# Kernel tuning notes

Measured on AMD Instinct MI355X. Metric: run time of the kernel, lower is better.

## Reference

```python
import jax, jax.numpy as jnp
import numpy as np
from functools import partial

NUM_ITERS = 3
NUM_CAPS = 8      # primary capsule count
NUM_CLASSES = 10
OUT_CH = 16       # digit capsule dim
INPUT_SIZE = 32 * 6 * 6  # 1152 primary capsule units per capsule map


def squash(s, axis=-1):
    # faithful to non_linear_squashing: s * (||s||^2/(1+||s||^2)) / (||s||+1e-10)
    norm_sqr = jnp.sum(s * s, axis=axis, keepdims=True)
    scale = jnp.sqrt(norm_sqr) + 1e-10
    mag = norm_sqr / (1.0 + norm_sqr)
    return s * mag / scale


def conv2d(x, w, b, stride):
    y = jax.lax.conv_general_dilated(
        x, w, window_strides=(stride, stride), padding='VALID',
        dimension_numbers=('NCHW', 'OIHW', 'NCHW'))
    return y + b[None, :, None, None]


def setup_inputs() -> dict:
    key = jax.random.key(0)
    ks = jax.random.split(key, 6)
    B = 256
    x = jax.random.normal(ks[0], (B, 1, 28, 28), dtype=jnp.float32)
    conv_w = jax.random.normal(ks[1], (256, 1, 9, 9), dtype=jnp.float32) * 0.05
    conv_b = jax.random.normal(ks[2], (256,), dtype=jnp.float32) * 0.05
    # 8 primary capsule conv units (256->32 each) fused into one 256->256 conv
    prim_w = jax.random.normal(ks[3], (NUM_CAPS * 32, 256, 9, 9), dtype=jnp.float32) * 0.02
    prim_b = jax.random.normal(ks[4], (NUM_CAPS * 32,), dtype=jnp.float32) * 0.02
    # digit routing weights (input_size, num_classes, out_channels, num_capsules)
    digit_w = jax.random.normal(ks[5], (INPUT_SIZE, NUM_CLASSES, OUT_CH, NUM_CAPS), dtype=jnp.float32)
    return {'x': x, 'conv_w': conv_w, 'conv_b': conv_b,
            'prim_w': prim_w, 'prim_b': prim_b, 'digit_w': digit_w}


def reference(x, conv_w, conv_b, prim_w, prim_b, digit_w):
    B = x.shape[0]
    # conv stack: 1->256 k9 s1 + ReLU  (28 -> 20); pool is MaxPool2d(1,1) = identity
    h = jax.nn.relu(conv2d(x, conv_w, conv_b, stride=1))  # (B,256,20,20)
    # primary capsules: 8 convs 256->32 k9 s2, no activation (nl_activation=False)
    p = conv2d(h, prim_w, prim_b, stride=2)               # (B,256,6,6)
    u = p.reshape(B, NUM_CAPS, -1)                        # (B,8,1152)
    u = squash(u, axis=-1)
    # digit layer with dynamic routing
    # u_i: (B, IS, 8);  u_j_i[b,i,c,o] = sum_k W[i,c,o,k] * u_i[b,i,k]
    u_i = jnp.transpose(u, (0, 2, 1))                     # (B,1152,8)
    u_j_i = jnp.einsum('icok,bik->bico', digit_w, u_i)    # (B,1152,10,16)
    b_ij = jnp.zeros((INPUT_SIZE, NUM_CLASSES), dtype=x.dtype)
    out = None
    for _ in range(NUM_ITERS):
        c_ij = jax.nn.softmax(b_ij, axis=0)               # softmax over input capsules (dim=1 in torch)
        s_j = jnp.einsum('ic,bico->bco', c_ij, u_j_i)     # (B,10,16)
        # original squashes (B,1,C,16,1) along dim=2 == the CLASS axis
        out = squash(s_j, axis=1)                         # (B,10,16)
        # agreement: mean over batch of <u_j_i, v_j>
        u_v = jnp.einsum('bico,bco->ic', u_j_i, out) / B  # (1152,10)
        b_ij = b_ij + u_v
    # torch returns out.squeeze(1) with shape (B, C, 16, 1)
    return out[..., None]
```

## Files before the change

### kernel.cpp

```cpp
#include <hip/hip_runtime.h>
#include <cstdint>
#include <cstddef>


typedef __attribute__((ext_vector_type(8))) short short8;
typedef __attribute__((ext_vector_type(4))) float f32x4;

#define PHALF 2359296

__device__ __forceinline__ unsigned short f2bf_rn(float x) {
    unsigned u = __float_as_uint(x);
    unsigned r = (u + 0x7fffu + ((u >> 16) & 1u)) >> 16;
    return (unsigned short)r;
}

__global__ void k_makew(const float* __restrict__ w2,
                        unsigned short* __restrict__ wt) {
    __shared__ float lw[20736];
    int ocg = blockIdx.x, icg = blockIdx.y, t = threadIdx.x;
    for (int idx = t; idx < 20736; idx += 256) {
        int row = idx / 81, k = idx % 81;
        int oc_l = row >> 5, ic_l = row & 31;
        lw[idx] = w2[((size_t)(ocg * 8 + oc_l) * 256 + icg * 32 + ic_l) * 81 + k];
    }
    __syncthreads();
    for (int idx = t; idx < 2592; idx += 256) {
        int k = idx >> 5;
        int r = idx & 31;
        int oc_l = r >> 2, sl = r & 3;
        unsigned short hi8[8];
        #pragma unroll
        for (int j = 0; j < 8; j++)
            hi8[j] = f2bf_rn(lw[(oc_l * 32 + sl * 8 + j) * 81 + k]);
        size_t o = ((size_t)(k * 256 + ocg * 8 + oc_l)) * 256 + icg * 32 + sl * 8;
        *(uint4*)&wt[o] = *(uint4*)hi8;
    }
}

__global__ void k_conv1(const float* __restrict__ x, const float* __restrict__ cw,
                        const float* __restrict__ cb,
                        unsigned short* __restrict__ h) {
    __shared__ float img[784];
    __shared__ float wsm[32 * 81];
    int b = blockIdx.x, ocg = blockIdx.y, t = threadIdx.x;
    for (int idx = t; idx < 784; idx += 256) img[idx] = x[b * 784 + idx];
    for (int idx = t; idx < 2592; idx += 256) wsm[idx] = cw[ocg * 2592 + idx];
    __syncthreads();
    int oc_l = t & 31, g = t >> 5;
    int oc = ocg * 32 + oc_l;
    float bias = cb[oc];
    const float* wp = &wsm[oc_l * 81];
    for (int q = g; q < 100; q += 8) {
        int py = q / 5, qx = (q % 5) * 4;
        float a0 = bias, a1 = bias, a2 = bias, a3 = bias;
        #pragma unroll
        for (int ky = 0; ky < 9; ky++) {
            const float* ir = &img[(py + ky) * 28 + qx];
            float r[12];
            #pragma unroll
            for (int j = 0; j < 12; j++) r[j] = ir[j];
            #pragma unroll
            for (int kx = 0; kx < 9; kx++) {
                float w = wp[ky * 9 + kx];
                a0 += r[kx] * w; a1 += r[kx + 1] * w;
                a2 += r[kx + 2] * w; a3 += r[kx + 3] * w;
            }
        }
        float v[4] = { fmaxf(a0, 0.f), fmaxf(a1, 0.f), fmaxf(a2, 0.f), fmaxf(a3, 0.f) };
        size_t base = ((size_t)b * 400 + py * 20 + qx) * 256 + oc;
        #pragma unroll
        for (int j = 0; j < 4; j++)
            h[base + (size_t)j * 256] = f2bf_rn(v[j]);
    }
}

__global__ __launch_bounds__(256, 4) void k_conv2m(
    const unsigned short* __restrict__ h,
    const unsigned short* __restrict__ wt,
    float* __restrict__ p0, float* __restrict__ p1,
    float* __restrict__ p2, float* __restrict__ p3)
{
    __shared__ unsigned short smem[14336];
    const int t = threadIdx.x;
    const int w = t >> 6, l = t & 63;
    const int mb = blockIdx.x, nb = blockIdx.y, zz = blockIdx.z;
    const int half = zz >> 1, seg = zz & 1;

    const unsigned short* src;
    int nld, sbase;
    unsigned rowbase[4];
    const bool isA = (w < 2);
    if (isA) {
        src = h; nld = 3; sbase = w * 1536;
        #pragma unroll
        for (int ld = 0; ld < 3; ld++) {
            int L = w * 24 + ld * 8 + (l >> 3);
            int p = l & 7;
            int tt = p ^ (L & 7);
            int s = tt >> 2, qc = tt & 3;
            int row = L * 2 + s;
            int P = mb * 96 + row;
            int b = P / 36, o = P % 36;
            int oy = o / 6, ox = o % 6;
            rowbase[ld] = (unsigned)((b * 400 + oy * 40 + ox * 2) * 256 + half * 128 + qc * 8);
        }
    } else {
        src = wt; nld = 4; sbase = 3072 + (w - 2) * 2048;
        #pragma unroll
        for (int ld = 0; ld < 4; ld++) {
            int L = (w - 2) * 32 + ld * 8 + (l >> 3);
            int p = l & 7;
            int tt = p ^ (L & 7);
            int s = tt >> 2, qc = tt & 3;
            int oc = L * 2 + s;
            rowbase[ld] = (unsigned)((nb * 128 + oc) * 256 + half * 128 + qc * 8);
        }
    }

    const int wm = w & 1, wn = w >> 1;
    const int lane16 = l & 15, q = l >> 4;

    f32x4 acc[3][4] = {};

    const int pos0 = seg ? 41 : 0;
    const int npos = seg ? 40 : 41;
    const int NR = npos * 4;

    auto kofs_of = [&](int sr) -> unsigned {
        int pos = pos0 + (sr >> 2), q32 = sr & 3;
        if (isA) {
            int ky = pos / 9, kx = pos - ky * 9;
            return (unsigned)((ky * 20 + kx) * 256 + q32 * 32);
        }
        return (unsigned)(pos * 65536 + q32 * 32);
    };
    auto stage = [&](int bf, unsigned kofs) {
        for (int ld = 0; ld < nld; ld++) {
            __builtin_amdgcn_global_load_lds(
                (const __attribute__((address_space(1))) unsigned int*)(const void*)(src + rowbase[ld] + kofs),
                (__attribute__((address_space(3))) unsigned int*)(void*)(smem + bf * 7168 + sbase + ld * 512),
                16, 0, 0);
        }
    };
    auto compute = [&](int bf) {
        const unsigned short* bufp = smem + bf * 7168;
        short8 a[3], b[4];
        #pragma unroll
        for (int mt = 0; mt < 3; mt++) {
            int r = wm * 48 + mt * 16 + lane16;
            int L = r >> 1;
            int p = (((r & 1) << 2) + q) ^ (L & 7);
            a[mt] = *(const short8*)(bufp + L * 64 + p * 8);
        }
        #pragma unroll
        for (int nt = 0; nt < 4; nt++) {
            int r = wn * 64 + nt * 16 + lane16;
            int L = r >> 1;
            int p = (((r & 1) << 2) + q) ^ (L & 7);
            b[nt] = *(const short8*)(bufp + 3072 + L * 64 + p * 8);
        }
        #pragma unroll
        for (int mt = 0; mt < 3; mt++)
            #pragma unroll
            for (int nt = 0; nt < 4; nt++)
                acc[mt][nt] = __builtin_amdgcn_mfma_f32_16x16x32_bf16(a[mt], b[nt], acc[mt][nt], 0, 0, 0);
    };

    stage(0, kofs_of(0));
    __syncthreads();
    int cur = 0;
    for (int sr = 0; sr < NR - 1; ++sr) {
        stage(cur ^ 1, kofs_of(sr + 1));
        compute(cur);
        __syncthreads();
        cur ^= 1;
    }
    compute(cur);

    #pragma unroll
    for (int mt = 0; mt < 3; mt++) {
        int pixG = mb * 96 + wm * 48 + mt * 16 + q * 4;
        int b = pixG / 36, p36 = pixG % 36;
        #pragma unroll
        for (int nt = 0; nt < 4; nt++) {
            int oc = nb * 128 + wn * 64 + nt * 16 + lane16;
            float* pout = (zz == 0) ? p0 : (zz == 1) ? p1 : (zz == 2) ? p2 : p3;
            *(f32x4*)&pout[((size_t)(b * 256 + oc)) * 36 + p36] = acc[mt][nt];
        }
    }
}

__global__ void k_squash1(const float* __restrict__ q0, const float* __restrict__ q1,
                          const float* __restrict__ q2, const float* __restrict__ q3,
                          const float* __restrict__ prim_b, float* __restrict__ U) {
    __shared__ float red[4];
    int b = blockIdx.x >> 3, cap = blockIdx.x & 7;
    int t = threadIdx.x;
    size_t base = ((size_t)b * 256 + cap * 32) * 36;
    const float* pa = q0 + base;
    const float* pb = q1 + base;
    const float* pc = q2 + base;
    const float* pd = q3 + base;
    float v[5];
    float ss = 0.f;
    #pragma unroll
    for (int j = 0; j < 5; j++) {
        int idx = t + j * 256;
        if (idx < 1152) {
            int ch_l = idx / 36;
            float val = pa[idx] + pb[idx] + pc[idx] + pd[idx] + prim_b[cap * 32 + ch_l];
            v[j] = val; ss += val * val;
        } else v[j] = 0.f;
    }
    for (int off = 32; off; off >>= 1) ss += __shfl_down(ss, off);
    if ((t & 63) == 0) red[t >> 6] = ss;
    __syncthreads();
    float n2 = red[0] + red[1] + red[2] + red[3];
    float f = (n2 / (1.0f + n2)) / (sqrtf(n2) + 1e-10f);
    #pragma unroll
    for (int j = 0; j < 5; j++) {
        int idx = t + j * 256;
        if (idx < 1152) U[(size_t)b * 9216 + idx * 8 + cap] = v[j] * f;
    }
}

__global__ void k_dwt2(const float* __restrict__ dw, float* __restrict__ dwT2) {
    int co = blockIdx.x, t = threadIdx.x;
    int c = co >> 4, o = co & 15;
    const float* base = dw + c * 128 + o * 8;
    float* out = dwT2 + (size_t)co * 9216;
    for (int idx = t; idx < 9216; idx += 256) {
        int i = idx >> 3, k = idx & 7;
        out[idx] = base[(size_t)i * 1280 + k];
    }
}

__global__ void k_ut(const float* __restrict__ U, float* __restrict__ UT) {
    __shared__ float tl[64][65];
    int ikb = blockIdx.x, bb = blockIdx.y, t = threadIdx.x;
    for (int idx = t; idx < 1024; idx += 256) {
        int row = idx >> 4, c4 = idx & 15;
        float4 v = *(const float4*)&U[(size_t)(bb * 64 + row) * 9216 + ikb * 64 + c4 * 4];
        tl[c4 * 4 + 0][row] = v.x;
        tl[c4 * 4 + 1][row] = v.y;
        tl[c4 * 4 + 2][row] = v.z;
        tl[c4 * 4 + 3][row] = v.w;
    }
    __syncthreads();
    for (int idx = t; idx < 1024; idx += 256) {
        int row = idx >> 4, c4 = idx & 15;
        float4 v = make_float4(tl[row][c4 * 4 + 0], tl[row][c4 * 4 + 1],
                               tl[row][c4 * 4 + 2], tl[row][c4 * 4 + 3]);
        *(float4*)&UT[(size_t)(ikb * 64 + row) * 256 + bb * 64 + c4 * 4] = v;
    }
}

__global__ void k_softmax(const float* __restrict__ bij, float* __restrict__ csm) {
    __shared__ float red[4];
    int c = blockIdx.x, t = threadIdx.x;
    float vals[5];
    float mx = -1e30f;
    #pragma unroll
    for (int j = 0; j < 5; j++) {
        int i = t + j * 256;
        vals[j] = (i < 1152) ? bij[i * 10 + c] : -1e30f;
        mx = fmaxf(mx, vals[j]);
    }
    for (int off = 32; off; off >>= 1) mx = fmaxf(mx, __shfl_down(mx, off));
    if ((t & 63) == 0) red[t >> 6] = mx;
    __syncthreads();
    mx = fmaxf(fmaxf(red[0], red[1]), fmaxf(red[2], red[3]));
    __syncthreads();
    float s = 0.f;
    #pragma unroll
    for (int j = 0; j < 5; j++) {
        int i = t + j * 256;
        vals[j] = (i < 1152) ? expf(vals[j] - mx) : 0.f;
        s += vals[j];
    }
    for (int off = 32; off; off >>= 1) s += __shfl_down(s, off);
    if ((t & 63) == 0) red[t >> 6] = s;
    __syncthreads();
    s = red[0] + red[1] + red[2] + red[3];
    float inv = 1.0f / s;
    #pragma unroll
    for (int j = 0; j < 5; j++) {
        int i = t + j * 256;
        if (i < 1152) csm[i * 10 + c] = vals[j] * inv;
    }
}

__global__ __launch_bounds__(256) void k_gemm1(const float* __restrict__ U,
                                               const float* __restrict__ dwT2,
                                               const float* __restrict__ csm,
                                               float* __restrict__ part,
                                               int uniform) {
    __shared__ float Us[32 * 36];
    __shared__ float WsT[5120];
    __shared__ float cl[360];
    int mb = blockIdx.x, kc = blockIdx.y, t = threadIdx.x;
    int tc = t & 15, tb = t >> 4;
    if (!uniform)
        for (int idx = t; idx < 360; idx += 256) cl[idx] = csm[kc * 360 + idx];
    const float uscale = 1.0f / 1152.0f;
    float acc[2][10] = {};
    for (int ks = 0; ks < 9; ks++) {
        __syncthreads();
        {
            int bb = t >> 3, k4 = t & 7;
            *(float4*)&Us[bb * 36 + k4 * 4] =
                *(const float4*)&U[(size_t)(mb * 32 + bb) * 9216 + kc * 288 + ks * 32 + k4 * 4];
        }
        #pragma unroll
        for (int pass = 0; pass < 5; pass++) {
            int s = t + pass * 256;
            int co = s >> 3, p = s & 7;
            int kq = p ^ (co & 7);
            int ikl = ks * 32 + kq * 4;
            float4 v = *(const float4*)&dwT2[(size_t)co * 9216 + kc * 288 + ikl];
            float sc = uniform ? uscale : cl[(ikl >> 3) * 10 + (co >> 4)];
            v.x *= sc; v.y *= sc; v.z *= sc; v.w *= sc;
            *(float4*)&WsT[s * 4] = v;
        }
        __syncthreads();
        float a0[32], a1[32];
        #pragma unroll
        for (int kq = 0; kq < 8; kq++) {
            float4 v0 = *(const float4*)&Us[(tb * 2) * 36 + kq * 4];
            float4 v1 = *(const float4*)&Us[(tb * 2 + 1) * 36 + kq * 4];
            a0[kq * 4 + 0] = v0.x; a0[kq * 4 + 1] = v0.y; a0[kq * 4 + 2] = v0.z; a0[kq * 4 + 3] = v0.w;
            a1[kq * 4 + 0] = v1.x; a1[kq * 4 + 1] = v1.y; a1[kq * 4 + 2] = v1.z; a1[kq * 4 + 3] = v1.w;
        }
        #pragma unroll
        for (int j = 0; j < 10; j++) {
            int co = tc + 16 * j;
            int cx = co & 7, cbase = co * 32;
            #pragma unroll
            for (int kq = 0; kq < 8; kq++) {
                float4 wv = *(const float4*)&WsT[cbase + ((kq ^ cx) << 2)];
                acc[0][j] += a0[kq * 4 + 0] * wv.x; acc[0][j] += a0[kq * 4 + 1] * wv.y;
                acc[0][j] += a0[kq * 4 + 2] * wv.z; acc[0][j] += a0[kq * 4 + 3] * wv.w;
                acc[1][j] += a1[kq * 4 + 0] * wv.x; acc[1][j] += a1[kq * 4 + 1] * wv.y;
                acc[1][j] += a1[kq * 4 + 2] * wv.z; acc[1][j] += a1[kq * 4 + 3] * wv.w;
            }
        }
    }
    #pragma unroll
    for (int r = 0; r < 2; r++)
        #pragma unroll
        for (int j = 0; j < 10; j++)
            part[(size_t)kc * 40960 + (mb * 32 + tb * 2 + r) * 160 + tc + 16 * j] = acc[r][j];
}

__global__ void k_redsq(const float* __restrict__ part, float* __restrict__ out,
                        float* __restrict__ outT, int writeT) {
    __shared__ float sl[160];
    __shared__ float n2s[16];
    int b = blockIdx.x, t = threadIdx.x;
    float s = 0.f;
    if (t < 160) {
        for (int kc = 0; kc < 32; kc++) s += part[(size_t)kc * 40960 + b * 160 + t];
        sl[t] = s;
    }
    __syncthreads();
    if (t < 16) {
        float n2 = 0.f;
        #pragma unroll
        for (int c = 0; c < 10; c++) { float v = sl[c * 16 + t]; n2 += v * v; }
        n2s[t] = n2;
    }
    __syncthreads();
    if (t < 160) {
        float n2 = n2s[t & 15];
        float f = (n2 / (1.0f + n2)) / (sqrtf(n2) + 1e-10f);
        float r = s * f;
        out[(size_t)b * 160 + t] = r;
        if (writeT) outT[(size_t)t * 256 + b] = r;
    }
}

__global__ __launch_bounds__(256) void k_g2uv(const float* __restrict__ UT,
                                              const float* __restrict__ outTg,
                                              const float* __restrict__ dw,
                                              float* __restrict__ bij) {
    __shared__ float UsT[1024];
    __shared__ float OsT[5120];
    __shared__ float dwl[5120];
    __shared__ float sb[320];
    int blk = blockIdx.x, t = threadIdx.x;
    int tc = t & 15, tm = t >> 4;
    for (int idx = t; idx < 5120; idx += 256)
        dwl[idx] = dw[(size_t)blk * 5120 + idx];
    float acc[2][10] = {};
    for (int bs = 0; bs < 256; bs += 32) {
        __syncthreads();
        {
            int m = t >> 3, p = t & 7;
            int kq = p ^ (m & 7);
            *(float4*)&UsT[t * 4] =
                *(const float4*)&UT[(size_t)(blk * 32 + m) * 256 + bs + kq * 4];
        }
        #pragma unroll
        for (int pass = 0; pass < 5; pass++) {
            int s = t + pass * 256;
            int co = s >> 3, p = s & 7;
            int kq = p ^ (co & 7);
            *(float4*)&OsT[s * 4] =
                *(const float4*)&outTg[(size_t)co * 256 + bs + kq * 4];
        }
        __syncthreads();
        float a0[32], a1[32];
        int m0 = tm * 2, m1 = tm * 2 + 1;
        #pragma unroll
        for (int kq = 0; kq < 8; kq++) {
            float4 v0 = *(const float4*)&UsT[m0 * 32 + ((kq ^ (m0 & 7)) << 2)];
            float4 v1 = *(const float4*)&UsT[m1 * 32 + ((kq ^ (m1 & 7)) << 2)];
            a0[kq * 4 + 0] = v0.x; a0[kq * 4 + 1] = v0.y; a0[kq * 4 + 2] = v0.z; a0[kq * 4 + 3] = v0.w;
            a1[kq * 4 + 0] = v1.x; a1[kq * 4 + 1] = v1.y; a1[kq * 4 + 2] = v1.z; a1[kq * 4 + 3] = v1.w;
        }
        #pragma unroll
        for (int j = 0; j < 10; j++) {
            int co = tc + 16 * j;
            int cx = co & 7, cbase = co * 32;
            #pragma unroll
            for (int kq = 0; kq < 8; kq++) {
                float4 wv = *(const float4*)&OsT[cbase + ((kq ^ cx) << 2)];
                acc[0][j] += a0[kq * 4 + 0] * wv.x; acc[0][j] += a0[kq * 4 + 1] * wv.y;
                acc[0][j] += a0[kq * 4 + 2] * wv.z; acc[0][j] += a0[kq * 4 + 3] * wv.w;
                acc[1][j] += a1[kq * 4 + 0] * wv.x; acc[1][j] += a1[kq * 4 + 1] * wv.y;
                acc[1][j] += a1[kq * 4 + 2] * wv.z; acc[1][j] += a1[kq * 4 + 3] * wv.w;
            }
        }
    }
    #pragma unroll
    for (int r = 0; r < 2; r++) {
        int ik_l = tm * 2 + r;
        int i_l = ik_l >> 3, k = ik_l & 7;
        #pragma unroll
        for (int j = 0; j < 10; j++) {
            float v = acc[r][j] * dwl[i_l * 1280 + (j * 16 + tc) * 8 + k];
            v += __shfl_down(v, 8, 16);
            v += __shfl_down(v, 4, 16);
            v += __shfl_down(v, 2, 16);
            v += __shfl_down(v, 1, 16);
            if (tc == 0) sb[ik_l * 10 + j] = v;
        }
    }
    __syncthreads();
    if (t < 40) {
        int i_l = t / 10, c = t % 10;
        float s = 0.f;
        #pragma unroll
        for (int kk = 0; kk < 8; kk++) s += sb[(i_l * 8 + kk) * 10 + c];
        size_t o = (size_t)(blk * 4 + i_l) * 10 + c;
        bij[o] += s * (1.0f / 256.0f);
    }
}

extern "C" void kernel_launch(void* const* d_in, const int* in_sizes, int n_in,
                              void* d_out, int out_size, void* d_ws, size_t ws_size,
                              hipStream_t stream) {
    const float* x      = (const float*)d_in[0];
    const float* conv_w = (const float*)d_in[1];
    const float* conv_b = (const float*)d_in[2];
    const float* prim_w = (const float*)d_in[3];
    const float* prim_b = (const float*)d_in[4];
    const float* dw     = (const float*)d_in[5];

    char* wsb = (char*)d_ws;
    unsigned short* h  = (unsigned short*)(wsb);
    unsigned short* wt = (unsigned short*)(wsb + 52428800);
    float* pp0  = (float*)(wsb + 63045632);
    float* pp1  = (float*)(wsb + 72482816);
    float* U    = (float*)(wsb + 81920000);
    float* dwT2 = (float*)(wsb + 91357184);
    float* pp3  = (float*)(wsb + 91357184);
    float* part = (float*)(wsb + 97255424);
    float* csm  = (float*)(wsb + 102498304);
    float* bij  = (float*)(wsb + 102544384);
    float* outT = (float*)(wsb + 102590464);
    float* outw = (float*)(wsb + 102754304);
    float* UT   = (float*)(wsb + 102918144);
    float* pp2  = (float*)(wsb + 102918144);

    k_makew<<<dim3(32, 8), 256, 0, stream>>>(prim_w, wt);
    k_conv1<<<dim3(256, 8), 256, 0, stream>>>(x, conv_w, conv_b, h);
    k_conv2m<<<dim3(96, 2, 4), 256, 0, stream>>>(h, wt, pp0, pp1, pp2, pp3);
    k_squash1<<<2048, 256, 0, stream>>>(pp0, pp1, pp2, pp3, prim_b, U);
    k_dwt2<<<160, 256, 0, stream>>>(dw, dwT2);
    k_ut<<<dim3(144, 4), 256, 0, stream>>>(U, UT);
    hipMemsetAsync(bij, 0, 11520 * sizeof(float), stream);

    k_gemm1<<<dim3(8, 32), 256, 0, stream>>>(U, dwT2, csm, part, 1);
    k_redsq<<<256, 256, 0, stream>>>(part, outw, outT, 1);
    k_g2uv<<<288, 256, 0, stream>>>(UT, outT, dw, bij);
    k_softmax<<<10, 256, 0, stream>>>(bij, csm);
    k_gemm1<<<dim3(8, 32), 256, 0, stream>>>(U, dwT2, csm, part, 0);
    k_redsq<<<256, 256, 0, stream>>>(part, outw, outT, 1);
    k_g2uv<<<288, 256, 0, stream>>>(UT, outT, dw, bij);
    k_softmax<<<10, 256, 0, stream>>>(bij, csm);
    k_gemm1<<<dim3(8, 32), 256, 0, stream>>>(U, dwT2, csm, part, 0);
    k_redsq<<<256, 256, 0, stream>>>(part, (float*)d_out, outT, 0);
}
```

Before: 508.7 us.

## Triple-buffer conv2 LDS staging with manual vmcnt waits and MFMA priority

```diff
diff --git a/kernel.cpp b/kernel.cpp
--- a/kernel.cpp
+++ b/kernel.cpp
@@ -80,7 +80,7 @@
     float* __restrict__ p0, float* __restrict__ p1,
     float* __restrict__ p2, float* __restrict__ p3)
 {
-    __shared__ unsigned short smem[14336];
+    __shared__ unsigned short smem[21504];
     const int t = threadIdx.x;
     const int w = t >> 6, l = t & 63;
     const int mb = blockIdx.x, nb = blockIdx.y, zz = blockIdx.z;
@@ -135,10 +135,11 @@
         return (unsigned)(pos * 65536 + q32 * 32);
     };
     auto stage = [&](int bf, unsigned kofs) {
+        unsigned short* dst = smem + bf * 7168 + sbase;
         for (int ld = 0; ld < nld; ld++) {
             __builtin_amdgcn_global_load_lds(
                 (const __attribute__((address_space(1))) unsigned int*)(const void*)(src + rowbase[ld] + kofs),
-                (__attribute__((address_space(3))) unsigned int*)(void*)(smem + bf * 7168 + sbase + ld * 512),
+                (__attribute__((address_space(3))) unsigned int*)(void*)(dst + ld * 512),
                 16, 0, 0);
         }
     };
@@ -159,23 +160,48 @@
             int p = (((r & 1) << 2) + q) ^ (L & 7);
             b[nt] = *(const short8*)(bufp + 3072 + L * 64 + p * 8);
         }
+        __builtin_amdgcn_s_setprio(1);
         #pragma unroll
         for (int mt = 0; mt < 3; mt++)
             #pragma unroll
             for (int nt = 0; nt < 4; nt++)
                 acc[mt][nt] = __builtin_amdgcn_mfma_f32_16x16x32_bf16(a[mt], b[nt], acc[mt][nt], 0, 0, 0);
+        __builtin_amdgcn_s_setprio(0);
     };
 
+    #define BARRIER() asm volatile("s_barrier" ::: "memory")
+    #define WAIT_2NLD() do { if (isA) asm volatile("s_waitcnt vmcnt(6)" ::: "memory"); \
+                             else     asm volatile("s_waitcnt vmcnt(8)" ::: "memory"); } while (0)
+    #define WAIT_1NLD() do { if (isA) asm volatile("s_waitcnt vmcnt(3)" ::: "memory"); \
+                             else     asm volatile("s_waitcnt vmcnt(4)" ::: "memory"); } while (0)
+    #define WAIT_0()    asm volatile("s_waitcnt vmcnt(0)" ::: "memory")
+
     stage(0, kofs_of(0));
-    __syncthreads();
-    int cur = 0;
-    for (int sr = 0; sr < NR - 1; ++sr) {
-        stage(cur ^ 1, kofs_of(sr + 1));
-        compute(cur);
-        __syncthreads();
-        cur ^= 1;
-    }
-    compute(cur);
+    stage(1, kofs_of(1));
+
+    int bc = 0;
+    int st = 2;
+    for (int sr = 0; sr < NR - 2; ++sr) {
+        stage(st, kofs_of(sr + 2));
+        WAIT_2NLD();
+        BARRIER();
+        compute(bc);
+        BARRIER();
+        bc = (bc == 2) ? 0 : bc + 1;
+        st = (st == 2) ? 0 : st + 1;
+    }
+    WAIT_1NLD();
+    BARRIER();
+    compute(bc);
+    bc = (bc == 2) ? 0 : bc + 1;
+    WAIT_0();
+    BARRIER();
+    compute(bc);
+
+    #undef BARRIER
+    #undef WAIT_2NLD
+    #undef WAIT_1NLD
+    #undef WAIT_0
 
     #pragma unroll
     for (int mt = 0; mt < 3; mt++) {
```

Result: no change. 504.1 us (-0.9%).
